# Optimization experiments

Hardware: AMD Instinct MI355X
Metric: run time of the kernel (lower is better)

The kernel has to match this reference:

```python
import jax, jax.numpy as jnp
import numpy as np

V, P, D, H, L, FF = 40478, 512, 768, 12, 12, 4 * 768
EPS = 1e-5


def setup_inputs() -> dict:
    key = jax.random.key(0)
    ks = jax.random.split(key, 16)
    s = 0.02
    inp = {
        "input_ids": jax.random.randint(ks[0], (8, 512), 0, V, dtype=jnp.int32),
        "attention_mask": jnp.ones((8, 512), dtype=jnp.int32),
        "tok_emb": jax.random.normal(ks[1], (V, D), jnp.float32) * s,
        "pos_emb": jax.random.normal(ks[2], (P, D), jnp.float32) * s,
        "Wqkv": jax.random.normal(ks[3], (L, D, 3 * D), jnp.float32) * s,
        "bqkv": jnp.zeros((L, 3 * D), jnp.float32),
        "Wo": jax.random.normal(ks[4], (L, D, D), jnp.float32) * s,
        "bo": jnp.zeros((L, D), jnp.float32),
        "ln1_g": jnp.ones((L, D), jnp.float32),
        "ln1_b": jnp.zeros((L, D), jnp.float32),
        "Wfc": jax.random.normal(ks[5], (L, D, FF), jnp.float32) * s,
        "bfc": jnp.zeros((L, FF), jnp.float32),
        "Wp2": jax.random.normal(ks[6], (L, FF, D), jnp.float32) * s,
        "bp2": jnp.zeros((L, D), jnp.float32),
        "ln2_g": jnp.ones((L, D), jnp.float32),
        "ln2_b": jnp.zeros((L, D), jnp.float32),
    }
    return inp


def _layernorm(x, g, b):
    m = jnp.mean(x, axis=-1, keepdims=True)
    v = jnp.mean(jnp.square(x - m), axis=-1, keepdims=True)
    return (x - m) * jax.lax.rsqrt(v + EPS) * g + b


def _forward(input_ids, attention_mask, tok_emb, pos_emb, Wqkv, bqkv, Wo, bo,
             ln1_g, ln1_b, Wfc, bfc, Wp2, bp2, ln2_g, ln2_b):
    B, S = input_ids.shape
    dh = D // H
    h = tok_emb[input_ids] + pos_emb[jnp.arange(S)][None, :, :]  # [B,S,D]
    # additive attention mask: (1 - m) * -10000, broadcast to [B,1,1,S]
    amask = (1.0 - attention_mask.astype(h.dtype))[:, None, None, :] * -10000.0
    # causal mask b: 1s in lower triangle; w = w*b - 10000*(1-b)
    causal = (jnp.arange(S)[:, None] >= jnp.arange(S)[None, :]).astype(h.dtype)  # [S,S]

    def block(h, p):
        Wqkv_, bqkv_, Wo_, bo_, g1, b1, Wfc_, bfc_, Wp2_, bp2_, g2, b2 = p
        qkv = h @ Wqkv_ + bqkv_                                   # [B,S,3D]
        q, k, v = jnp.split(qkv, 3, axis=-1)
        q = q.reshape(B, S, H, dh).transpose(0, 2, 1, 3)          # [B,H,S,dh]
        k = k.reshape(B, S, H, dh).transpose(0, 2, 1, 3)
        v = v.reshape(B, S, H, dh).transpose(0, 2, 1, 3)
        w = jnp.einsum('bhqd,bhkd->bhqk', q, k) / jnp.sqrt(jnp.asarray(dh, h.dtype))
        w = w * causal - 10000.0 * (1.0 - causal) + amask
        w = jax.nn.softmax(w, axis=-1)
        a = jnp.einsum('bhqk,bhkd->bhqd', w, v)                   # [B,H,S,dh]
        a = a.transpose(0, 2, 1, 3).reshape(B, S, D)
        a = a @ Wo_ + bo_
        n = _layernorm(h + a, g1, b1)
        m = jax.nn.gelu(n @ Wfc_ + bfc_) @ Wp2_ + bp2_
        return _layernorm(n + m, g2, b2), None

    params = (Wqkv, bqkv, Wo, bo, ln1_g, ln1_b, Wfc, bfc, Wp2, bp2, ln2_g, ln2_b)
    h, _ = jax.lax.scan(block, h, params)
    return h


def reference(input_ids, attention_mask, tok_emb, pos_emb, Wqkv, bqkv, Wo, bo,
              ln1_g, ln1_b, Wfc, bfc, Wp2, bp2, ln2_g, ln2_b):
    return _forward(input_ids, attention_mask, tok_emb, pos_emb, Wqkv, bqkv, Wo, bo,
                    ln1_g, ln1_b, Wfc, bfc, Wp2, bp2, ln2_g, ln2_b)
```

## Files before the change

### kernel.cpp

```cpp
#include <hip/hip_runtime.h>


typedef unsigned short u16;
typedef unsigned int u32;
typedef __bf16 bf16x8 __attribute__((ext_vector_type(8)));
typedef float f32x4 __attribute__((ext_vector_type(4)));

__device__ __forceinline__ float bf2f(u16 u) {
    union { unsigned int i; float f; } c; c.i = ((unsigned int)u) << 16; return c.f;
}
__device__ __forceinline__ u16 f2bf(float f) {
    union { float f; unsigned int i; } c; c.f = f;
    unsigned int b = c.i;
    return (u16)((b + 0x7fffu + ((b >> 16) & 1u)) >> 16);
}
__device__ __forceinline__ float gelu_f(float x) {
    float y = 0.7978845608028654f * (x + 0.044715f * x * x * x);
    float t = __expf(2.0f * y);
    float th = 1.0f - 2.0f / (t + 1.0f);
    return 0.5f * x * (1.0f + th);
}
__device__ __forceinline__ void async_cp16(const u16* g, u16* l) {
    __builtin_amdgcn_global_load_lds(
        (const __attribute__((address_space(1))) u32*)g,
        (__attribute__((address_space(3))) u32*)l, 16, 0, 0);
}

template<int BM, int BN, int WR, int WC, int EPI>
__global__ __launch_bounds__(256) void gemm_k(
    const u16* __restrict__ A, int lda, long long aSB, long long aSH,
    const u16* __restrict__ Bt, int ldb, long long bSB, long long bSH,
    void* __restrict__ Cv, int ldc, long long cSB, long long cSH,
    const float* __restrict__ bias, const float* __restrict__ res,
    const int* __restrict__ amask,
    int K, int Hh)
{
    constexpr int BK = 64;
    constexpr int WM = BM / WR, WN = BN / WC;
    constexpr int FM = WM / 16, FN = WN / 16;
    __shared__ __align__(16) u16 As[BM * BK];
    __shared__ __align__(16) u16 Bs[BN * BK];
    const int t = threadIdx.x;
    const int lane = t & 63;
    const int w = t >> 6;
    const int wr = w / WC, wc = w % WC;
    const int zb = blockIdx.z / Hh, zh = blockIdx.z % Hh;
    const u16* Ab = A + zb * aSB + zh * aSH + (size_t)blockIdx.x * BM * lda;
    const u16* Bb = Bt + zb * bSB + zh * bSH + (size_t)blockIdx.y * BN * ldb;

    f32x4 acc[FM][FN];
#pragma unroll
    for (int i = 0; i < FM; ++i)
#pragma unroll
        for (int j = 0; j < FN; ++j)
            acc[i][j] = (f32x4){0.f, 0.f, 0.f, 0.f};

    for (int k0 = 0; k0 < K; k0 += BK) {
        __syncthreads();
#pragma unroll
        for (int p = 0; p < (BM * BK) / 2048; ++p) {
            int idx8 = p * 256 + t;
            int grp = idx8 >> 6, l6 = idx8 & 63;
            int row = (grp >> 1) * 16 + (l6 & 15);
            int k = (grp & 1) * 32 + (l6 >> 4) * 8;
            int base8 = p * 256 + (t & ~63);
            async_cp16(Ab + (size_t)row * lda + k0 + k, &As[(size_t)base8 * 8]);
        }
#pragma unroll
        for (int p = 0; p < (BN * BK) / 2048; ++p) {
            int idx8 = p * 256 + t;
            int grp = idx8 >> 6, l6 = idx8 & 63;
            int row = (grp >> 1) * 16 + (l6 & 15);
            int k = (grp & 1) * 32 + (l6 >> 4) * 8;
            int base8 = p * 256 + (t & ~63);
            async_cp16(Bb + (size_t)row * ldb + k0 + k, &Bs[(size_t)base8 * 8]);
        }
        __syncthreads();
#pragma unroll
        for (int ks = 0; ks < 2; ++ks) {
            bf16x8 aF[FM], bF[FN];
#pragma unroll
            for (int i = 0; i < FM; ++i) {
                int gA = (wr * WM) / 16 + i;
                aF[i] = *(const bf16x8*)(&As[((gA * 2 + ks) * 64 + lane) * 8]);
            }
#pragma unroll
            for (int j = 0; j < FN; ++j) {
                int gB = (wc * WN) / 16 + j;
                bF[j] = *(const bf16x8*)(&Bs[((gB * 2 + ks) * 64 + lane) * 8]);
            }
#pragma unroll
            for (int i = 0; i < FM; ++i)
#pragma unroll
                for (int j = 0; j < FN; ++j)
                    acc[i][j] = __builtin_amdgcn_mfma_f32_16x16x32_bf16(
                        aF[i], bF[j], acc[i][j], 0, 0, 0);
        }
    }

    const int q = lane >> 4, cn = lane & 15;
#pragma unroll
    for (int i = 0; i < FM; ++i) {
#pragma unroll
        for (int j = 0; j < FN; ++j) {
            int mBase = blockIdx.x * BM + wr * WM + i * 16 + q * 4;
            int n0 = blockIdx.y * BN + wc * WN + j * 16 + cn;
#pragma unroll
            for (int r = 0; r < 4; ++r) {
                int m = mBase + r;
                float v = acc[i][j][r];
                if constexpr (EPI == 0) {
                    float* Cp = (float*)Cv + zb * cSB + zh * cSH;
                    Cp[(size_t)m * ldc + n0] = v;
                } else if constexpr (EPI == 1) {
                    if (bias) v += bias[n0];
                    u16* Cp = (u16*)Cv + zb * cSB + zh * cSH;
                    Cp[(size_t)m * ldc + n0] = f2bf(v);
                } else if constexpr (EPI == 3) {
                    v += bias[n0];
                    v = gelu_f(v);
                    u16* Cp = (u16*)Cv + zb * cSB + zh * cSH;
                    Cp[(size_t)m * ldc + n0] = f2bf(v);
                } else {
                    v += bias[n0] + res[(size_t)m * ldc + n0];
                    float* Cp = (float*)Cv + zb * cSB + zh * cSH;
                    Cp[(size_t)m * ldc + n0] = v;
                }
            }
        }
    }
}

__global__ __launch_bounds__(256) void transpose_w_k(
    const float* __restrict__ src, u16* __restrict__ dst, int K, int N)
{
    __shared__ float tile[32][33];
    const int n0 = blockIdx.x * 32, k0 = blockIdx.y * 32;
    const size_t zoff = (size_t)blockIdx.z * K * N;
    src += zoff;
    dst += zoff;
    const int tx = threadIdx.x & 31, ty = threadIdx.x >> 5;
#pragma unroll
    for (int i = 0; i < 4; ++i) {
        int k = k0 + ty + i * 8;
        tile[ty + i * 8][tx] = src[(size_t)k * N + n0 + tx];
    }
    __syncthreads();
#pragma unroll
    for (int i = 0; i < 4; ++i) {
        int n = n0 + ty + i * 8;
        dst[(size_t)n * K + k0 + tx] = f2bf(tile[tx][ty + i * 8]);
    }
}

__global__ __launch_bounds__(256) void vtrans_k(
    const u16* __restrict__ qkv, u16* __restrict__ vt)
{
    __shared__ u16 tile[32][66];
    const int z = blockIdx.y;
    const int b = z / 12, h = z % 12;
    const int jc = blockIdx.x * 32;
    const int d = threadIdx.x & 63, jj = threadIdx.x >> 6;
    const u16* src = qkv + (size_t)b * 512 * 2304 + 1536 + (size_t)h * 64;
#pragma unroll
    for (int i = 0; i < 8; ++i) {
        int j = jc + jj + i * 4;
        tile[jj + i * 4][d] = src[(size_t)j * 2304 + d];
    }
    __syncthreads();
    const int jx = threadIdx.x & 31, dd0 = threadIdx.x >> 5;
    u16* dstz = vt + (size_t)z * 64 * 512;
#pragma unroll
    for (int i = 0; i < 8; ++i) {
        int dd = dd0 + i * 8;
        dstz[(size_t)dd * 512 + jc + jx] = tile[jx][dd];
    }
}

__global__ __launch_bounds__(256) void fattn_k(
    const u16* __restrict__ qkv, const u16* __restrict__ vt,
    u16* __restrict__ out, const int* __restrict__ amask)
{
    __shared__ __align__(16) u16 Qs[32 * 64];
    __shared__ __align__(16) u16 KVs[2][64 * 64];
    __shared__ __align__(16) u16 Ps[32 * 512];
    __shared__ float red[4][32];

    const int t = threadIdx.x;
    const int lane = t & 63;
    const int w = t >> 6;
    const int q4 = lane >> 4, cn = lane & 15;
    const int z = blockIdx.x;
    const int b = z / 12, h = z % 12;
    const int x = 15 - (int)blockIdx.y;
    const int q0 = x * 32;
    const int nch = (q0 + 32 + 63) >> 6;

    const u16* Qg = qkv + (size_t)(b * 512 + q0) * 2304 + h * 64;
    const u16* Kg = qkv + (size_t)(b * 512) * 2304 + 768 + h * 64;
    const u16* Vg = vt + (size_t)z * 64 * 512;

    {
        int grp = t >> 6, l6 = t & 63;
        int row = (grp >> 1) * 16 + (l6 & 15);
        int k = (grp & 1) * 32 + (l6 >> 4) * 8;
        int base8 = t & ~63;
        async_cp16(Qg + (size_t)row * 2304 + k, &Qs[base8 * 8]);
    }
    auto stageK = [&](int c, int buf) {
#pragma unroll
        for (int p = 0; p < 2; ++p) {
            int idx8 = p * 256 + t;
            int grp = idx8 >> 6, l6 = idx8 & 63;
            int row = (grp >> 1) * 16 + (l6 & 15);
            int k = (grp & 1) * 32 + (l6 >> 4) * 8;
            int base8 = p * 256 + (t & ~63);
            async_cp16(Kg + (size_t)(c * 64 + row) * 2304 + k,
                       &KVs[buf][base8 * 8]);
        }
    };
    auto stageV = [&](int c, int buf) {
#pragma unroll
        for (int p = 0; p < 2; ++p) {
            int idx8 = p * 256 + t;
            int grp = idx8 >> 6, l6 = idx8 & 63;
            int row = (grp >> 1) * 16 + (l6 & 15);
            int k = (grp & 1) * 32 + (l6 >> 4) * 8;
            int base8 = p * 256 + (t & ~63);
            async_cp16(Vg + (size_t)row * 512 + c * 64 + k,
                       &KVs[buf][base8 * 8]);
        }
    };
    stageK(0, 0);
    __syncthreads();

    bf16x8 qF[2][2];
#pragma unroll
    for (int i = 0; i < 2; ++i)
#pragma unroll
        for (int ks = 0; ks < 2; ++ks)
            qF[i][ks] = *(const bf16x8*)(&Qs[((i * 2 + ks) * 64 + lane) * 8]);

    f32x4 acc[2][8];
#pragma unroll
    for (int i = 0; i < 2; ++i)
#pragma unroll
        for (int c = 0; c < 8; ++c)
            acc[i][c] = (f32x4){0.f, 0.f, 0.f, 0.f};

#pragma unroll
    for (int c = 0; c < 8; ++c) {
        if (c < nch) {
            if (c + 1 < nch) stageK(c + 1, (c + 1) & 1);
            else stageV(0, nch & 1);
            const u16* Kb = KVs[c & 1];
#pragma unroll
            for (int ks = 0; ks < 2; ++ks) {
                bf16x8 bF = *(const bf16x8*)(&Kb[((w * 2 + ks) * 64 + lane) * 8]);
#pragma unroll
                for (int i = 0; i < 2; ++i)
                    acc[i][c] = __builtin_amdgcn_mfma_f32_16x16x32_bf16(
                        qF[i][ks], bF, acc[i][c], 0, 0, 0);
            }
            __syncthreads();
        }
    }

    float mx[2][4];
#pragma unroll
    for (int i = 0; i < 2; ++i)
#pragma unroll
        for (int r = 0; r < 4; ++r) mx[i][r] = -1e30f;
#pragma unroll
    for (int c = 0; c < 8; ++c) {
        if (c < nch) {
            int j = c * 64 + w * 16 + cn;
            float am = (1.0f - (float)amask[b * 512 + j]) * -10000.0f;
#pragma unroll
            for (int i = 0; i < 2; ++i)
#pragma unroll
                for (int r = 0; r < 4; ++r) {
                    int q = q0 + i * 16 + q4 * 4 + r;
                    float s = (j <= q) ? (acc[i][c][r] * 0.125f + am)
                                       : (-10000.0f + am);
                    acc[i][c][r] = s;
                    mx[i][r] = fmaxf(mx[i][r], s);
                }
        }
    }
#pragma unroll
    for (int i = 0; i < 2; ++i)
#pragma unroll
        for (int r = 0; r < 4; ++r) {
            float m = mx[i][r];
            m = fmaxf(m, __shfl_xor(m, 1));
            m = fmaxf(m, __shfl_xor(m, 2));
            m = fmaxf(m, __shfl_xor(m, 4));
            m = fmaxf(m, __shfl_xor(m, 8));
            mx[i][r] = m;
        }
    if (cn == 0) {
#pragma unroll
        for (int i = 0; i < 2; ++i)
#pragma unroll
            for (int r = 0; r < 4; ++r)
                red[w][i * 16 + q4 * 4 + r] = mx[i][r];
    }
    __syncthreads();
#pragma unroll
    for (int i = 0; i < 2; ++i)
#pragma unroll
        for (int r = 0; r < 4; ++r) {
            int q = i * 16 + q4 * 4 + r;
            mx[i][r] = fmaxf(fmaxf(red[0][q], red[1][q]),
                             fmaxf(red[2][q], red[3][q]));
        }
    __syncthreads();

    float sm[2][4];
#pragma unroll
    for (int i = 0; i < 2; ++i)
#pragma unroll
        for (int r = 0; r < 4; ++r) sm[i][r] = 0.f;
#pragma unroll
    for (int c = 0; c < 8; ++c) {
        if (c < nch) {
            int j = c * 64 + w * 16 + cn;
#pragma unroll
            for (int i = 0; i < 2; ++i)
#pragma unroll
                for (int r = 0; r < 4; ++r) {
                    float p = __expf(acc[i][c][r] - mx[i][r]);
                    sm[i][r] += p;
                    int row = i * 16 + q4 * 4 + r;
                    int sw = (row & 7) ^ ((row >> 3) & 1);
                    Ps[row * 512 + (j ^ (sw << 3))] = f2bf(p);
                }
        }
    }
#pragma unroll
    for (int i = 0; i < 2; ++i)
#pragma unroll
        for (int r = 0; r < 4; ++r) {
            float s = sm[i][r];
            s += __shfl_xor(s, 1);
            s += __shfl_xor(s, 2);
            s += __shfl_xor(s, 4);
            s += __shfl_xor(s, 8);
            sm[i][r] = s;
        }
    if (cn == 0) {
#pragma unroll
        for (int i = 0; i < 2; ++i)
#pragma unroll
            for (int r = 0; r < 4; ++r)
                red[w][i * 16 + q4 * 4 + r] = sm[i][r];
    }
    __syncthreads();
    float inv[2][4];
#pragma unroll
    for (int i = 0; i < 2; ++i)
#pragma unroll
        for (int r = 0; r < 4; ++r) {
            int q = i * 16 + q4 * 4 + r;
            inv[i][r] = 1.0f / (red[0][q] + red[1][q] + red[2][q] + red[3][q]);
        }

    f32x4 acc2[2];
    acc2[0] = (f32x4){0.f, 0.f, 0.f, 0.f};
    acc2[1] = (f32x4){0.f, 0.f, 0.f, 0.f};
#pragma unroll
    for (int c = 0; c < 8; ++c) {
        if (c < nch) {
            if (c + 1 < nch) stageV(c + 1, (nch + c + 1) & 1);
            const u16* Vb = KVs[(nch + c) & 1];
#pragma unroll
            for (int ks = 0; ks < 2; ++ks) {
                bf16x8 vF = *(const bf16x8*)(&Vb[((w * 2 + ks) * 64 + lane) * 8]);
                int jb = c * 64 + ks * 32 + q4 * 8;
#pragma unroll
                for (int i = 0; i < 2; ++i) {
                    int prow = i * 16 + cn;
                    int sw = (prow & 7) ^ ((prow >> 3) & 1);
                    bf16x8 pF = *(const bf16x8*)(
                        &Ps[prow * 512 + (jb ^ (sw << 3))]);
                    acc2[i] = __builtin_amdgcn_mfma_f32_16x16x32_bf16(
                        pF, vF, acc2[i], 0, 0, 0);
                }
            }
            __syncthreads();
        }
    }

#pragma unroll
    for (int i = 0; i < 2; ++i)
#pragma unroll
        for (int r = 0; r < 4; ++r) {
            int q = q0 + i * 16 + q4 * 4 + r;
            out[(size_t)(b * 512 + q) * 768 + h * 64 + w * 16 + cn] =
                f2bf(acc2[i][r] * inv[i][r]);
        }
}

template<int NP>
__global__ __launch_bounds__(256) void reduce_ln_k(
    const float* __restrict__ parts, const float* __restrict__ bias,
    const float* __restrict__ res, const float* __restrict__ g,
    const float* __restrict__ b, float* __restrict__ out, u16* __restrict__ outb)
{
    __shared__ float red[4];
    const int r = blockIdx.x, t = threadIdx.x;
    const size_t base = (size_t)r * 768;
    float v[3];
#pragma unroll
    for (int i = 0; i < 3; ++i) {
        const int d = t + i * 256;
        float x = res[base + d] + bias[d];
#pragma unroll
        for (int p = 0; p < NP; ++p)
            x += parts[(size_t)p * 4096 * 768 + base + d];
        v[i] = x;
    }
    float s = v[0] + v[1] + v[2];
    for (int o = 1; o < 64; o <<= 1) s += __shfl_xor(s, o);
    if ((t & 63) == 0) red[t >> 6] = s;
    __syncthreads();
    const float mean = (red[0] + red[1] + red[2] + red[3]) * (1.0f / 768.0f);
    __syncthreads();
    float d0 = v[0] - mean, d1 = v[1] - mean, d2 = v[2] - mean;
    float s2 = d0 * d0 + d1 * d1 + d2 * d2;
    for (int o = 1; o < 64; o <<= 1) s2 += __shfl_xor(s2, o);
    if ((t & 63) == 0) red[t >> 6] = s2;
    __syncthreads();
    const float var = (red[0] + red[1] + red[2] + red[3]) * (1.0f / 768.0f);
    const float rs = rsqrtf(var + 1e-5f);
    float y0 = d0 * rs * g[t] + b[t];
    float y1 = d1 * rs * g[t + 256] + b[t + 256];
    float y2 = d2 * rs * g[t + 512] + b[t + 512];
    out[base + t] = y0; out[base + t + 256] = y1; out[base + t + 512] = y2;
    outb[base + t] = f2bf(y0);
    outb[base + t + 256] = f2bf(y1);
    outb[base + t + 512] = f2bf(y2);
}

__global__ __launch_bounds__(256) void embed_k(
    const int* __restrict__ ids, const float* __restrict__ tok,
    const float* __restrict__ pos, float* __restrict__ h, u16* __restrict__ hb)
{
    const int e = blockIdx.x * 256 + threadIdx.x;
    const int r = e / 768, d = e - r * 768;
    const int srow = r & 511;
    const int id = ids[r];
    const float v = tok[(size_t)id * 768 + d] + pos[(size_t)srow * 768 + d];
    h[e] = v;
    hb[e] = f2bf(v);
}

extern "C" void kernel_launch(void* const* d_in, const int* in_sizes, int n_in,
                              void* d_out, int out_size, void* d_ws, size_t ws_size,
                              hipStream_t stream)
{
    (void)in_sizes; (void)n_in; (void)out_size; (void)ws_size;
    const int*   ids  = (const int*)d_in[0];
    const int*   mask = (const int*)d_in[1];
    const float* tok  = (const float*)d_in[2];
    const float* pos  = (const float*)d_in[3];
    const float* Wqkv = (const float*)d_in[4];
    const float* bqkv = (const float*)d_in[5];
    const float* Wo   = (const float*)d_in[6];
    const float* bo   = (const float*)d_in[7];
    const float* g1   = (const float*)d_in[8];
    const float* b1   = (const float*)d_in[9];
    const float* Wfc  = (const float*)d_in[10];
    const float* bfc  = (const float*)d_in[11];
    const float* Wp2  = (const float*)d_in[12];
    const float* bp2  = (const float*)d_in[13];
    const float* g2   = (const float*)d_in[14];
    const float* b2   = (const float*)d_in[15];

    char* ws = (char*)d_ws;
    size_t off = 0;
    auto alloc = [&](size_t elems, size_t esz) {
        void* p = ws + off;
        off += (elems * esz + 255) & ~(size_t)255;
        return p;
    };
    u16*   WqkvT  = (u16*)alloc(12ull * 2304 * 768, 2);
    u16*   WoT    = (u16*)alloc(12ull * 768 * 768, 2);
    u16*   WfcT   = (u16*)alloc(12ull * 3072 * 768, 2);
    u16*   Wp2T   = (u16*)alloc(12ull * 768 * 3072, 2);
    float* h      = (float*)alloc(4096ull * 768, 4);
    u16*   hb     = (u16*)alloc(4096ull * 768, 2);
    u16*   qkvb   = (u16*)alloc(4096ull * 2304, 2);
    u16*   scores = (u16*)alloc(96ull * 512 * 512, 2);
    u16*   Vt     = (u16*)alloc(96ull * 64 * 512, 2);
    u16*   attnb  = (u16*)alloc(4096ull * 768, 2);
    float* nbuf   = (float*)alloc(4096ull * 768, 4);
    u16*   nb     = (u16*)alloc(4096ull * 768, 2);
    u16*   fcb    = (u16*)alloc(4096ull * 3072, 2);
    float* P1 = (float*)fcb;
    float* P2 = (float*)scores;

    transpose_w_k<<<dim3(72, 24, 12), 256, 0, stream>>>(Wqkv, WqkvT, 768, 2304);
    transpose_w_k<<<dim3(24, 24, 12), 256, 0, stream>>>(Wo, WoT, 768, 768);
    transpose_w_k<<<dim3(96, 24, 12), 256, 0, stream>>>(Wfc, WfcT, 768, 3072);
    transpose_w_k<<<dim3(24, 96, 12), 256, 0, stream>>>(Wp2, Wp2T, 3072, 768);
    embed_k<<<12288, 256, 0, stream>>>(ids, tok, pos, h, hb);

    for (int l = 0; l < 12; ++l) {
        gemm_k<128, 128, 2, 2, 1><<<dim3(32, 18, 1), 256, 0, stream>>>(
            hb, 768, 0, 0, WqkvT + (size_t)l * 2304 * 768, 768, 0, 0,
            qkvb, 2304, 0, 0, bqkv + l * 2304, nullptr, nullptr, 768, 1);
        vtrans_k<<<dim3(16, 96), 256, 0, stream>>>(qkvb, Vt);
        fattn_k<<<dim3(96, 16), 256, 0, stream>>>(qkvb, Vt, attnb, mask);
        gemm_k<128, 128, 2, 2, 0><<<dim3(32, 6, 2), 256, 0, stream>>>(
            attnb, 768, 0, 384, WoT + (size_t)l * 768 * 768, 768, 0, 384,
            P1, 768, 0, 4096LL * 768, nullptr, nullptr, nullptr, 384, 2);
        reduce_ln_k<2><<<4096, 256, 0, stream>>>(
            P1, bo + l * 768, h, g1 + l * 768, b1 + l * 768, nbuf, nb);
        gemm_k<128, 128, 2, 2, 3><<<dim3(32, 24, 1), 256, 0, stream>>>(
            nb, 768, 0, 0, WfcT + (size_t)l * 3072 * 768, 768, 0, 0,
            fcb, 3072, 0, 0, bfc + l * 3072, nullptr, nullptr, 768, 1);
        gemm_k<128, 128, 2, 2, 0><<<dim3(32, 6, 4), 256, 0, stream>>>(
            fcb, 3072, 0, 768, Wp2T + (size_t)l * 768 * 3072, 3072, 0, 768,
            P2, 768, 0, 4096LL * 768, nullptr, nullptr, nullptr, 768, 4);
        float* dsth = (l == 11) ? (float*)d_out : h;
        reduce_ln_k<4><<<4096, 256, 0, stream>>>(
            P2, bp2 + l * 768, nbuf, g2 + l * 768, b2 + l * 768, dsth, hb);
    }
}
```

Before: 3.507 ms.

## Replace GEMM with 256x256 double-buffered 8-wave kernel with phased prefetch

Swaps the 128x128 single-buffered 4-wave GEMM for a 256x256-tile kernel with 512 threads and double-buffered LDS. Async global-to-LDS loads for the next K tile are interleaved with MFMA phases, using raw barriers, explicit vmcnt waits and s_setprio. The goal is to hide global load latency and raise data reuse per tile. In exchange the grids are much smaller (for example 144 or 96 blocks, against 256 CUs), which risks leaving CUs idle, and the hand-written waitcnt schedule is fragile.

```diff
diff --git a/kernel.cpp b/kernel.cpp
--- a/kernel.cpp
+++ b/kernel.cpp
@@ -5,6 +5,9 @@
 typedef unsigned int u32;
 typedef __bf16 bf16x8 __attribute__((ext_vector_type(8)));
 typedef float f32x4 __attribute__((ext_vector_type(4)));
+
+#define RAW_BAR() asm volatile("s_barrier" ::: "memory")
+#define WAITV(N) asm volatile("s_waitcnt vmcnt(" #N ")" ::: "memory")
 
 __device__ __forceinline__ float bf2f(u16 u) {
     union { unsigned int i; float f; } c; c.i = ((unsigned int)u) << 16; return c.f;
@@ -26,105 +29,129 @@
         (__attribute__((address_space(3))) u32*)l, 16, 0, 0);
 }
 
-template<int BM, int BN, int WR, int WC, int EPI>
-__global__ __launch_bounds__(256) void gemm_k(
-    const u16* __restrict__ A, int lda, long long aSB, long long aSH,
-    const u16* __restrict__ Bt, int ldb, long long bSB, long long bSH,
-    void* __restrict__ Cv, int ldc, long long cSB, long long cSH,
-    const float* __restrict__ bias, const float* __restrict__ res,
-    const int* __restrict__ amask,
-    int K, int Hh)
-{
-    constexpr int BK = 64;
-    constexpr int WM = BM / WR, WN = BN / WC;
-    constexpr int FM = WM / 16, FN = WN / 16;
-    __shared__ __align__(16) u16 As[BM * BK];
-    __shared__ __align__(16) u16 Bs[BN * BK];
+template<int EPI>
+__global__ __launch_bounds__(512, 2) void gemm256_k(
+    const u16* __restrict__ A, int lda, int aStep,
+    const u16* __restrict__ Bt, int ldb, int bStep,
+    void* __restrict__ Cv, int ldc, long long cStep,
+    const float* __restrict__ bias, int K)
+{
+    __shared__ __align__(16) u16 As[2][2][128 * 64];
+    __shared__ __align__(16) u16 Bs[2][2][128 * 64];
     const int t = threadIdx.x;
     const int lane = t & 63;
     const int w = t >> 6;
-    const int wr = w / WC, wc = w % WC;
-    const int zb = blockIdx.z / Hh, zh = blockIdx.z % Hh;
-    const u16* Ab = A + zb * aSB + zh * aSH + (size_t)blockIdx.x * BM * lda;
-    const u16* Bb = Bt + zb * bSB + zh * bSH + (size_t)blockIdx.y * BN * ldb;
-
-    f32x4 acc[FM][FN];
-#pragma unroll
-    for (int i = 0; i < FM; ++i)
-#pragma unroll
-        for (int j = 0; j < FN; ++j)
-            acc[i][j] = (f32x4){0.f, 0.f, 0.f, 0.f};
-
-    for (int k0 = 0; k0 < K; k0 += BK) {
-        __syncthreads();
-#pragma unroll
-        for (int p = 0; p < (BM * BK) / 2048; ++p) {
-            int idx8 = p * 256 + t;
+    const int wr = w >> 2, wc = w & 3;
+    const int s = blockIdx.z;
+    const u16* Ab = A + (size_t)blockIdx.x * 256 * lda + (size_t)s * aStep;
+    const u16* Bb = Bt + (size_t)blockIdx.y * 256 * ldb + (size_t)s * bStep;
+    const int nkt = K >> 6;
+
+    auto stage_half = [&](u16* dst, const u16* src, int ld, int k0) {
+#pragma unroll
+        for (int p = 0; p < 2; ++p) {
+            int idx8 = p * 512 + t;
             int grp = idx8 >> 6, l6 = idx8 & 63;
             int row = (grp >> 1) * 16 + (l6 & 15);
             int k = (grp & 1) * 32 + (l6 >> 4) * 8;
-            int base8 = p * 256 + (t & ~63);
-            async_cp16(Ab + (size_t)row * lda + k0 + k, &As[(size_t)base8 * 8]);
-        }
-#pragma unroll
-        for (int p = 0; p < (BN * BK) / 2048; ++p) {
-            int idx8 = p * 256 + t;
-            int grp = idx8 >> 6, l6 = idx8 & 63;
-            int row = (grp >> 1) * 16 + (l6 & 15);
-            int k = (grp & 1) * 32 + (l6 >> 4) * 8;
-            int base8 = p * 256 + (t & ~63);
-            async_cp16(Bb + (size_t)row * ldb + k0 + k, &Bs[(size_t)base8 * 8]);
-        }
-        __syncthreads();
-#pragma unroll
-        for (int ks = 0; ks < 2; ++ks) {
-            bf16x8 aF[FM], bF[FN];
-#pragma unroll
-            for (int i = 0; i < FM; ++i) {
-                int gA = (wr * WM) / 16 + i;
-                aF[i] = *(const bf16x8*)(&As[((gA * 2 + ks) * 64 + lane) * 8]);
+            int base8 = p * 512 + (t & ~63);
+            async_cp16(src + (size_t)row * ld + k0 + k, dst + base8 * 8);
+        }
+    };
+
+    stage_half(As[0][0], Ab, lda, 0);
+    stage_half(As[0][1], Ab + (size_t)128 * lda, lda, 0);
+    stage_half(Bs[0][0], Bb, ldb, 0);
+    stage_half(Bs[0][1], Bb + (size_t)128 * ldb, ldb, 0);
+    if (1 < nkt) {
+        stage_half(Bs[1][0], Bb, ldb, 64);
+        stage_half(Bs[1][1], Bb + (size_t)128 * ldb, ldb, 64);
+        WAITV(4);
+    } else {
+        WAITV(0);
+    }
+    RAW_BAR();
+
+    f32x4 acc[8][4];
+#pragma unroll
+    for (int m = 0; m < 8; ++m)
+#pragma unroll
+        for (int n = 0; n < 4; ++n)
+            acc[m][n] = (f32x4){0.f, 0.f, 0.f, 0.f};
+
+    for (int T = 0; T < nkt; ++T) {
+        const int buf = T & 1;
+        const u16* Ah = As[buf][wr];
+        const u16* Bh = Bs[buf][wc >> 1];
+        bf16x8 bF[4][2];
+#pragma unroll
+        for (int ph = 0; ph < 4; ++ph) {
+            bf16x8 aP[2][2];
+#pragma unroll
+            for (int mi = 0; mi < 2; ++mi)
+#pragma unroll
+                for (int ks = 0; ks < 2; ++ks)
+                    aP[mi][ks] = *(const bf16x8*)(
+                        &Ah[(((2 * ph + mi) * 2 + ks) * 64 + lane) * 8]);
+            if (ph == 0) {
+#pragma unroll
+                for (int n = 0; n < 4; ++n)
+#pragma unroll
+                    for (int ks = 0; ks < 2; ++ks)
+                        bF[n][ks] = *(const bf16x8*)(
+                            &Bh[((((wc & 1) * 4 + n) * 2 + ks) * 64 + lane) * 8]);
             }
-#pragma unroll
-            for (int j = 0; j < FN; ++j) {
-                int gB = (wc * WN) / 16 + j;
-                bF[j] = *(const bf16x8*)(&Bs[((gB * 2 + ks) * 64 + lane) * 8]);
+            if (ph < 2) {
+                if (T + 1 < nkt)
+                    stage_half(As[(T + 1) & 1][ph],
+                               Ab + (size_t)(ph * 128) * lda, lda, (T + 1) * 64);
+            } else {
+                if (T + 2 < nkt)
+                    stage_half(Bs[buf][ph - 2],
+                               Bb + (size_t)((ph - 2) * 128) * ldb, ldb,
+                               (T + 2) * 64);
             }
-#pragma unroll
-            for (int i = 0; i < FM; ++i)
-#pragma unroll
-                for (int j = 0; j < FN; ++j)
-                    acc[i][j] = __builtin_amdgcn_mfma_f32_16x16x32_bf16(
-                        aF[i], bF[j], acc[i][j], 0, 0, 0);
-        }
-    }
-
-    const int q = lane >> 4, cn = lane & 15;
-#pragma unroll
-    for (int i = 0; i < FM; ++i) {
-#pragma unroll
-        for (int j = 0; j < FN; ++j) {
-            int mBase = blockIdx.x * BM + wr * WM + i * 16 + q * 4;
-            int n0 = blockIdx.y * BN + wc * WN + j * 16 + cn;
+            RAW_BAR();
+            asm volatile("s_waitcnt lgkmcnt(0)" ::: "memory");
+            __builtin_amdgcn_s_setprio(1);
+#pragma unroll
+            for (int mi = 0; mi < 2; ++mi)
+#pragma unroll
+                for (int n = 0; n < 4; ++n)
+#pragma unroll
+                    for (int ks = 0; ks < 2; ++ks)
+                        acc[2 * ph + mi][n] = __builtin_amdgcn_mfma_f32_16x16x32_bf16(
+                            aP[mi][ks], bF[n][ks], acc[2 * ph + mi][n], 0, 0, 0);
+            __builtin_amdgcn_s_setprio(0);
+            if (ph == 3) {
+                if (T + 3 <= nkt) { WAITV(4); }
+                else if (T + 2 == nkt) { WAITV(0); }
+            }
+            RAW_BAR();
+        }
+    }
+
+    const int q4 = lane >> 4, cn = lane & 15;
+#pragma unroll
+    for (int m = 0; m < 8; ++m) {
+#pragma unroll
+        for (int n = 0; n < 4; ++n) {
+            int mBase = blockIdx.x * 256 + wr * 128 + m * 16 + q4 * 4;
+            int n0 = blockIdx.y * 256 + wc * 64 + n * 16 + cn;
 #pragma unroll
             for (int r = 0; r < 4; ++r) {
-                int m = mBase + r;
-                float v = acc[i][j][r];
+                int mm = mBase + r;
+                float v = acc[m][n][r];
                 if constexpr (EPI == 0) {
-                    float* Cp = (float*)Cv + zb * cSB + zh * cSH;
-                    Cp[(size_t)m * ldc + n0] = v;
+                    float* Cp = (float*)Cv + (size_t)s * cStep;
+                    Cp[(size_t)mm * ldc + n0] = v;
                 } else if constexpr (EPI == 1) {
-                    if (bias) v += bias[n0];
-                    u16* Cp = (u16*)Cv + zb * cSB + zh * cSH;
-                    Cp[(size_t)m * ldc + n0] = f2bf(v);
-                } else if constexpr (EPI == 3) {
+                    v += bias[n0];
+                    ((u16*)Cv)[(size_t)mm * ldc + n0] = f2bf(v);
+                } else {
                     v += bias[n0];
                     v = gelu_f(v);
-                    u16* Cp = (u16*)Cv + zb * cSB + zh * cSH;
-                    Cp[(size_t)m * ldc + n0] = f2bf(v);
-                } else {
-                    v += bias[n0] + res[(size_t)m * ldc + n0];
-                    float* Cp = (float*)Cv + zb * cSB + zh * cSH;
-                    Cp[(size_t)m * ldc + n0] = v;
+                    ((u16*)Cv)[(size_t)mm * ldc + n0] = f2bf(v);
                 }
             }
         }
@@ -508,22 +535,22 @@
     embed_k<<<12288, 256, 0, stream>>>(ids, tok, pos, h, hb);
 
     for (int l = 0; l < 12; ++l) {
-        gemm_k<128, 128, 2, 2, 1><<<dim3(32, 18, 1), 256, 0, stream>>>(
-            hb, 768, 0, 0, WqkvT + (size_t)l * 2304 * 768, 768, 0, 0,
-            qkvb, 2304, 0, 0, bqkv + l * 2304, nullptr, nullptr, 768, 1);
+        gemm256_k<1><<<dim3(16, 9, 1), 512, 0, stream>>>(
+            hb, 768, 0, WqkvT + (size_t)l * 2304 * 768, 768, 0,
+            qkvb, 2304, 0, bqkv + l * 2304, 768);
         vtrans_k<<<dim3(16, 96), 256, 0, stream>>>(qkvb, Vt);
         fattn_k<<<dim3(96, 16), 256, 0, stream>>>(qkvb, Vt, attnb, mask);
-        gemm_k<128, 128, 2, 2, 0><<<dim3(32, 6, 2), 256, 0, stream>>>(
-            attnb, 768, 0, 384, WoT + (size_t)l * 768 * 768, 768, 0, 384,
-            P1, 768, 0, 4096LL * 768, nullptr, nullptr, nullptr, 384, 2);
+        gemm256_k<0><<<dim3(16, 3, 2), 512, 0, stream>>>(
+            attnb, 768, 384, WoT + (size_t)l * 768 * 768, 768, 384,
+            P1, 768, 4096LL * 768, nullptr, 384);
         reduce_ln_k<2><<<4096, 256, 0, stream>>>(
             P1, bo + l * 768, h, g1 + l * 768, b1 + l * 768, nbuf, nb);
-        gemm_k<128, 128, 2, 2, 3><<<dim3(32, 24, 1), 256, 0, stream>>>(
-            nb, 768, 0, 0, WfcT + (size_t)l * 3072 * 768, 768, 0, 0,
-            fcb, 3072, 0, 0, bfc + l * 3072, nullptr, nullptr, 768, 1);
-        gemm_k<128, 128, 2, 2, 0><<<dim3(32, 6, 4), 256, 0, stream>>>(
-            fcb, 3072, 0, 768, Wp2T + (size_t)l * 768 * 3072, 3072, 0, 768,
-            P2, 768, 0, 4096LL * 768, nullptr, nullptr, nullptr, 768, 4);
+        gemm256_k<3><<<dim3(16, 12, 1), 512, 0, stream>>>(
+            nb, 768, 0, WfcT + (size_t)l * 3072 * 768, 768, 0,
+            fcb, 3072, 0, bfc + l * 3072, 768);
+        gemm256_k<0><<<dim3(16, 3, 4), 512, 0, stream>>>(
+            fcb, 3072, 768, Wp2T + (size_t)l * 768 * 3072, 3072, 768,
+            P2, 768, 4096LL * 768, nullptr, 768);
         float* dsth = (l == 11) ? (float*)d_out : h;
         reduce_ln_k<4><<<4096, 256, 0, stream>>>(
             P2, bp2 + l * 768, nbuf, g2 + l * 768, b2 + l * 768, dsth, hb);
```

After: 2.840 ms. -19.0%, faster.
